# Kernel optimization log

Hardware: AMD Instinct MI355X
Metric: run time of the kernel (lower is better)

Reference implementation:

```python
import jax, jax.numpy as jnp
import numpy as np

H_SIZE = 768
N_HEADS = 12
HEAD = H_SIZE // N_HEADS
INTER = 3072
N_LAYERS = 6
VOCAB = 65536
WIDTH = 512  # attention_width
EPS = 1e-6


def rmsnorm(x, w):
    return x * jax.lax.rsqrt(jnp.mean(x * x, axis=-1, keepdims=True) + EPS) * w


def rotate_every_two(x):
    # interleaved rotation: (x0,x1,x2,x3,...) -> (-x1,x0,-x3,x2,...)
    x1 = x[..., ::2]
    x2 = x[..., 1::2]
    return jnp.stack((-x2, x1), axis=-1).reshape(x.shape)


def fixed_pos_embedding(ages, dim):
    # ages: [B,S] float32 -> sin,cos: [B,S,1,dim]
    inv_freq = 1.0 / 10000 ** jnp.linspace(0.0, 2.0, dim // 2)
    t = ages[..., None] * inv_freq  # [B,S,dim//2]
    sin, cos = jnp.sin(t), jnp.cos(t)
    shp = ages.shape + (1, dim)
    sin = jnp.stack((sin, sin), axis=-1).reshape(shp)
    cos = jnp.stack((cos, cos), axis=-1).reshape(shp)
    return sin, cos


def local_attention(q, k, v, width):
    # causal local attention: query i attends to keys j with i-width < j <= i
    B, S, H, D = q.shape
    nb = S // width
    qb = q.reshape(B, nb, width, H, D)
    pad = ((0, 0), (width, 0), (0, 0), (0, 0))
    kp = jnp.pad(k, pad).reshape(B, nb + 1, width, H, D)
    vp = jnp.pad(v, pad).reshape(B, nb + 1, width, H, D)
    k2 = jnp.concatenate((kp[:, :-1], kp[:, 1:]), axis=2)  # [B,nb,2W,H,D]
    v2 = jnp.concatenate((vp[:, :-1], vp[:, 1:]), axis=2)
    scale = 1.0 / jnp.sqrt(jnp.asarray(D, q.dtype))
    scores = jnp.einsum('bnqhd,bnkhd->bnhqk', qb, k2) * scale
    qi = jnp.arange(width)[:, None]
    kj = jnp.arange(2 * width)[None, :]
    blk = jnp.arange(nb)[:, None, None]
    # global: i = b*W+qi, j = b*W - W + kj ; valid: j<=i, i-j<W, j>=0
    valid = (kj > qi) & (kj <= qi + width) & ((blk * width - width + kj) >= 0)
    scores = jnp.where(valid[None, :, None, :, :], scores, -jnp.inf)
    attn = jax.nn.softmax(scores, axis=-1)
    out = jnp.einsum('bnhqk,bnkhd->bnqhd', attn, v2)
    return out.reshape(B, S, H, D)


def encoder_layer(x, sin, cos, p):
    B, S, _ = x.shape
    xn = rmsnorm(x, p['norm_w'])
    qkv = (xn @ p['attn_W'] + p['attn_b']).reshape(B, S, 3, N_HEADS, HEAD)
    q = qkv[:, :, 0] * cos + rotate_every_two(qkv[:, :, 0]) * sin
    k = qkv[:, :, 1] * cos + rotate_every_two(qkv[:, :, 1]) * sin
    v = qkv[:, :, 2]
    attn = local_attention(q, k, v, WIDTH).reshape(B, S, H_SIZE)
    ff = jax.nn.gelu(xn @ p['in_W'] + p['in_b'], approximate=False)
    combined = jnp.concatenate((attn, ff), axis=-1)
    return combined @ p['out_W'] + p['out_b']


def setup_inputs() -> dict:
    key = jax.random.key(0)
    ks = jax.random.split(key, 10)
    B, S = 4, 2048
    std = 0.02
    tokens = jax.random.randint(ks[0], (B, S), 0, VOCAB, dtype=jnp.int64 if jax.config.jax_enable_x64 else jnp.int32)
    ages = jax.random.uniform(ks[1], (B, S), dtype=jnp.float32) * 1000.0
    embed = jax.random.normal(ks[2], (VOCAB, H_SIZE), jnp.float32) * std
    in_norm_w = jnp.ones((H_SIZE,), jnp.float32)
    out_norm_w = jnp.ones((H_SIZE,), jnp.float32)
    norm_w = jnp.ones((N_LAYERS, H_SIZE), jnp.float32)
    attn_W = jax.random.normal(ks[3], (N_LAYERS, H_SIZE, 3 * H_SIZE), jnp.float32) * std
    attn_b = jnp.zeros((N_LAYERS, 3 * H_SIZE), jnp.float32)
    in_W = jax.random.normal(ks[4], (N_LAYERS, H_SIZE, INTER), jnp.float32) * std
    in_b = jnp.zeros((N_LAYERS, INTER), jnp.float32)
    out_W = jax.random.normal(ks[5], (N_LAYERS, H_SIZE + INTER, H_SIZE), jnp.float32) * std
    out_b = jnp.zeros((N_LAYERS, H_SIZE), jnp.float32)
    return {'tokens': tokens, 'ages': ages, 'embed': embed,
            'in_norm_w': in_norm_w, 'out_norm_w': out_norm_w, 'norm_w': norm_w,
            'attn_W': attn_W, 'attn_b': attn_b, 'in_W': in_W, 'in_b': in_b,
            'out_W': out_W, 'out_b': out_b}


def reference(tokens, ages, embed, in_norm_w, out_norm_w, norm_w, attn_W, attn_b, in_W, in_b, out_W, out_b):
    x = embed[tokens]
    x = rmsnorm(x, in_norm_w)
    sin, cos = fixed_pos_embedding(ages, HEAD)
    params = {'norm_w': norm_w, 'attn_W': attn_W, 'attn_b': attn_b,
              'in_W': in_W, 'in_b': in_b, 'out_W': out_W, 'out_b': out_b}

    def step(h, p):
        return h + encoder_layer(h, sin, cos, p), None

    x, _ = jax.lax.scan(step, x, params)
    return rmsnorm(x, out_norm_w)
```

## Files before the change

### kernel.cpp

```cpp
#include <hip/hip_runtime.h>
#include <hip/hip_bf16.h>
#include <math.h>

#define H_SIZE 768
#define N_HEADS 12
#define HEAD 64
#define INTER 3072
#define N_LAYERS 6
#define BATCH 4
#define SEQ 2048
#define BS (BATCH*SEQ)
#define EPSV 1e-6f

typedef __attribute__((ext_vector_type(8))) short bf16x8;
typedef __attribute__((ext_vector_type(4))) float f32x4;
typedef unsigned short u16;

__device__ inline float bf2f(u16 v) {
    union { float f; unsigned u; } x; x.u = ((unsigned)v) << 16; return x.f;
}
__device__ inline u16 f2bf(float f) {
    union { float f; unsigned u; } x; x.f = f;
    unsigned u = x.u;
    return (u16)((u + 0x7FFFu + ((u >> 16) & 1u)) >> 16);
}

__device__ __forceinline__ void stage16(const u16* g, u16* ldsbase) {
    __builtin_amdgcn_global_load_lds((const __attribute__((address_space(1))) void*)g,
                                     (__attribute__((address_space(3))) void*)ldsbase,
                                     16, 0, 0);
}

__global__ void probe_kernel(const u16* __restrict__ embed, const int* __restrict__ tokens,
                             int* __restrict__ flags) {
    if (threadIdx.x == 0 && blockIdx.x == 0) {
        int good = 0, evenzero = 0;
        for (int i = 0; i < 128; i++) {
            u16 h = embed[i];
            int e = (h >> 7) & 0xFF;
            if (h == 0 || (e >= 87 && e <= 133)) good++;
            if ((i & 1) == 0 && h == 0) evenzero++;
        }
        flags[0] = (evenzero >= 48) ? 1 : ((good >= 110) ? 0 : 1);
        int z = 0;
        for (int i = 0; i < 64; i++) if (tokens[2 * i + 1] == 0) z++;
        flags[1] = (z >= 60) ? 1 : 0;
    }
}

__global__ __launch_bounds__(256) void sincos_kernel(const void* __restrict__ ages,
                                                     float* __restrict__ SIN,
                                                     float* __restrict__ COS,
                                                     const int* __restrict__ flags) {
    int idx = blockIdx.x * 256 + threadIdx.x;
    if (idx >= BS * 32) return;
    bool f32in = flags[0] != 0;
    int row = idx >> 5, f = idx & 31;
    float age = f32in ? ((const float*)ages)[row] : bf2f(((const u16*)ages)[row]);
    float inv = expf(-(2.0f * (float)f / 31.0f) * 9.210340371976184f);
    float t = age * inv;
    SIN[idx] = sinf(t);
    COS[idx] = cosf(t);
}

__global__ __launch_bounds__(256) void wtrans_kernel(const void* __restrict__ Wsrc,
                                                     u16* __restrict__ Wt,
                                                     int K, int N, size_t ltstride,
                                                     const int* __restrict__ flags) {
    __shared__ u16 tile[64][72];
    bool f32in = flags[0] != 0;
    int l = blockIdx.z;
    const float* W32 = (const float*)Wsrc + (size_t)l * K * N;
    const u16*   W16 = (const u16*)Wsrc + (size_t)l * K * N;
    u16* out = Wt + (size_t)l * ltstride;
    int k0 = blockIdx.y * 64, n0 = blockIdx.x * 64;
    int t = threadIdx.x;
    int kk = t >> 3, nn = (t & 7) * 8;
#pragma unroll
    for (int it = 0; it < 2; it++) {
        int kr = kk + it * 32;
        u16 tmp[8];
        if (f32in) {
            const float* src = W32 + (size_t)(k0 + kr) * N + n0 + nn;
            float4 f0 = *(const float4*)src, f1 = *(const float4*)(src + 4);
            tmp[0] = f2bf(f0.x); tmp[1] = f2bf(f0.y); tmp[2] = f2bf(f0.z); tmp[3] = f2bf(f0.w);
            tmp[4] = f2bf(f1.x); tmp[5] = f2bf(f1.y); tmp[6] = f2bf(f1.z); tmp[7] = f2bf(f1.w);
        } else {
            uint4 v = *(const uint4*)(W16 + (size_t)(k0 + kr) * N + n0 + nn);
            const u16* pv = (const u16*)&v;
#pragma unroll
            for (int i = 0; i < 8; i++) tmp[i] = pv[i];
        }
        *(uint4*)(&tile[kr][nn]) = *(const uint4*)tmp;
    }
    __syncthreads();
    int n = t >> 3, kq = (t & 7) * 8;
#pragma unroll
    for (int it = 0; it < 2; it++) {
        int nr = n + it * 32;
        u16 tmp[8];
#pragma unroll
        for (int i = 0; i < 8; i++) tmp[i] = tile[kq + i][nr];
        *(uint4*)(out + (size_t)(n0 + nr) * K + k0 + kq) = *(const uint4*)tmp;
    }
}

__global__ __launch_bounds__(256) void bias_conv_kernel(const void* __restrict__ ab,
                                                        const void* __restrict__ ib,
                                                        const void* __restrict__ ob,
                                                        u16* __restrict__ dst,
                                                        const int* __restrict__ flags) {
    int i = blockIdx.x * 256 + threadIdx.x;
    bool f32in = flags[0] != 0;
    const int A = 6 * 2304, B = 6 * 3072, C = 6 * 768;
    if (i < A) dst[i] = f32in ? f2bf(((const float*)ab)[i]) : ((const u16*)ab)[i];
    else if (i < A + B) { int j = i - A; dst[i] = f32in ? f2bf(((const float*)ib)[j]) : ((const u16*)ib)[j]; }
    else if (i < A + B + C) { int j = i - A - B; dst[i] = f32in ? f2bf(((const float*)ob)[j]) : ((const u16*)ob)[j]; }
}

__global__ __launch_bounds__(256) void embed_norm_kernel(const int* __restrict__ tokens,
                                                         const void* __restrict__ embed,
                                                         const void* __restrict__ wbase,
                                                         float* __restrict__ X,
                                                         const int* __restrict__ flags) {
    int row = blockIdx.x * 4 + (threadIdx.x >> 6);
    int lane = threadIdx.x & 63;
    bool f32in = flags[0] != 0;
    bool i64 = flags[1] != 0;
    int tok = i64 ? tokens[2 * row] : tokens[row];
    tok &= 65535;
    const u16* er16 = (const u16*)embed + (size_t)tok * H_SIZE;
    const float* er32 = (const float*)embed + (size_t)tok * H_SIZE;
    const u16* w16 = (const u16*)wbase;
    const float* w32 = (const float*)wbase;
    float v[12]; float ss = 0.f;
#pragma unroll
    for (int k = 0; k < 12; k++) {
        int i = lane + k * 64;
        float t = f32in ? er32[i] : bf2f(er16[i]);
        v[k] = t; ss += t * t;
    }
#pragma unroll
    for (int off = 1; off < 64; off <<= 1) ss += __shfl_xor(ss, off, 64);
    float scale = rsqrtf(ss * (1.0f / 768.0f) + EPSV);
#pragma unroll
    for (int k = 0; k < 12; k++) {
        int i = lane + k * 64;
        float wv = f32in ? w32[i] : bf2f(w16[i]);
        X[(size_t)row * H_SIZE + i] = v[k] * scale * wv;
    }
}

__global__ __launch_bounds__(256) void rmsnorm_kernel(const float* __restrict__ X,
                                                      const void* __restrict__ wbase, size_t woff,
                                                      void* __restrict__ Y, int outMode,
                                                      const int* __restrict__ flags) {
    int row = blockIdx.x * 4 + (threadIdx.x >> 6);
    int lane = threadIdx.x & 63;
    bool f32in = flags[0] != 0;
    const u16* w16 = (const u16*)wbase + woff;
    const float* w32 = (const float*)wbase + woff;
    const float* xr = X + (size_t)row * H_SIZE;
    float v[12]; float ss = 0.f;
#pragma unroll
    for (int k = 0; k < 12; k++) { v[k] = xr[lane + k * 64]; ss += v[k] * v[k]; }
#pragma unroll
    for (int off = 1; off < 64; off <<= 1) ss += __shfl_xor(ss, off, 64);
    float scale = rsqrtf(ss * (1.0f / 768.0f) + EPSV);
    bool of32 = outMode && f32in;
#pragma unroll
    for (int k = 0; k < 12; k++) {
        int i = lane + k * 64;
        float wv = f32in ? w32[i] : bf2f(w16[i]);
        float val = v[k] * scale * wv;
        if (of32) ((float*)Y)[(size_t)row * H_SIZE + i] = val;
        else      ((u16*)Y)[(size_t)row * H_SIZE + i] = f2bf(val);
    }
}

__global__ __launch_bounds__(512, 2)
void gemm_fused_kernel(const u16* __restrict__ A,
                       const u16* __restrict__ Wt,
                       const u16* __restrict__ abias,
                       const u16* __restrict__ bbias,
                       u16* __restrict__ qkvb,
                       u16* __restrict__ combb,
                       const float* __restrict__ SIN,
                       const float* __restrict__ COS) {
    const int K = H_SIZE;
    const int NT = K / 64;
    __shared__ u16 Al[2][256][64];
    __shared__ u16 Bl[2][256][64];
    const int tid = threadIdx.x;
    const int lane = tid & 63, wave = tid >> 6;
    const int wm = wave >> 2, wn = wave & 3;
    const int lm = lane & 15, g = lane >> 4;
    const int l8 = lane >> 3, l7 = lane & 7;

    const int nx = gridDim.x;
    const int mpx = gridDim.y >> 3;
    int linear = blockIdx.y * nx + blockIdx.x;
    const int xcd = linear & 7;
    int wch = linear >> 3;
    int n_idx = wch / mpx;
    int m_loc = wch - n_idx * mpx;
    const int m0 = (xcd * mpx + m_loc) * 256;
    const int n0 = n_idx * 256;

    f32x4 acc[8][4];
#pragma unroll
    for (int i = 0; i < 8; i++)
#pragma unroll
        for (int j = 0; j < 4; j++) acc[i][j] = (f32x4)0.0f;

    const int swc = (l7 ^ l8) * 8;
    const u16* gA = A  + (size_t)(m0 + wave * 8 + l8) * K + swc;
    const u16* gB = Wt + (size_t)(n0 + wave * 8 + l8) * K + swc;

    auto STAGE_HALF = [&](int bi, int t, int which) {
        int h = (which & 1) * 128;
        if (which < 2) {
            stage16(gA + (size_t)h * K + t * 64,        &Al[bi][h + wave * 8][0]);
            stage16(gA + (size_t)(h + 64) * K + t * 64, &Al[bi][h + wave * 8 + 64][0]);
        } else {
            stage16(gB + (size_t)h * K + t * 64,        &Bl[bi][h + wave * 8][0]);
            stage16(gB + (size_t)(h + 64) * K + t * 64, &Bl[bi][h + wave * 8 + 64][0]);
        }
    };

    bf16x8 af[4][2], bf[4][2];
    const int rowsw = (lm & 7);

    auto RD_A = [&](int bi, int mh) {
#pragma unroll
        for (int i = 0; i < 4; i++)
#pragma unroll
            for (int ks = 0; ks < 2; ks++)
                af[i][ks] = *(const bf16x8*)(&Al[bi][wm * 128 + mh * 64 + i * 16 + lm]
                                               [((ks * 4 + g) ^ rowsw) * 8]);
    };
    auto RD_B = [&](int bi, int nh) {
#pragma unroll
        for (int j = 0; j < 2; j++)
#pragma unroll
            for (int ks = 0; ks < 2; ks++)
                bf[nh * 2 + j][ks] = *(const bf16x8*)(&Bl[bi][wn * 64 + nh * 32 + j * 16 + lm]
                                                        [((ks * 4 + g) ^ rowsw) * 8]);
    };
    auto MM = [&](int mh, int nh) {
        __builtin_amdgcn_s_setprio(1);
#pragma unroll
        for (int i = 0; i < 4; i++)
#pragma unroll
            for (int j = 0; j < 2; j++)
#pragma unroll
                for (int ks = 0; ks < 2; ks++)
                    acc[mh * 4 + i][nh * 2 + j] = __builtin_amdgcn_mfma_f32_16x16x32_bf16(
                        af[i][ks], bf[nh * 2 + j][ks], acc[mh * 4 + i][nh * 2 + j], 0, 0, 0);
        __builtin_amdgcn_s_setprio(0);
    };

    STAGE_HALF(0, 0, 0); STAGE_HALF(0, 0, 1); STAGE_HALF(0, 0, 2); STAGE_HALF(0, 0, 3);

    auto ITER = [&](int t, int ct) {
        const int nb = ct ^ 1;
        const bool pf = (t + 1 < NT);
        asm volatile("s_waitcnt vmcnt(0)" ::: "memory");
        __builtin_amdgcn_s_barrier();
        if (pf) STAGE_HALF(nb, t + 1, 0);
        RD_A(ct, 0); RD_B(ct, 0);
        MM(0, 0);
        __builtin_amdgcn_s_barrier();
        if (pf) STAGE_HALF(nb, t + 1, 1);
        RD_B(ct, 1);
        MM(0, 1);
        __builtin_amdgcn_s_barrier();
        if (pf) STAGE_HALF(nb, t + 1, 2);
        RD_A(ct, 1);
        MM(1, 0);
        __builtin_amdgcn_s_barrier();
        if (pf) STAGE_HALF(nb, t + 1, 3);
        MM(1, 1);
        __builtin_amdgcn_s_barrier();
    };

    for (int tt = 0; tt < NT; tt += 2) {
        ITER(tt, 0);
        ITER(tt + 1, 1);
    }

#pragma unroll
    for (int i = 0; i < 8; i++) {
        int mbase = m0 + wm * 128 + i * 16 + g * 4;
#pragma unroll
        for (int j = 0; j < 4; j++) {
            int n = n0 + wn * 64 + j * 16 + lm;
            float bv = (n < 2304) ? bf2f(abias[n]) : bf2f(bbias[n - 2304]);
#pragma unroll
            for (int r = 0; r < 4; r++) {
                float v = acc[i][j][r] + bv;
                int mm = mbase + r;
                float p = __shfl_xor(v, 1);
                if (n < 2304) {
                    float outv = v;
                    if (n < 1536) {
                        int f = (n >> 1) & 31;
                        float c = COS[mm * 32 + f], s = SIN[mm * 32 + f];
                        outv = (n & 1) ? (v * c + p * s) : (v * c - p * s);
                    }
                    qkvb[(size_t)mm * 2304 + n] = f2bf(outv);
                } else {
                    float u = 0.7978845608f * (v + 0.044715f * v * v * v);
                    float e = __expf(2.0f * u);
                    float th = 1.0f - 2.0f / (e + 1.0f);
                    combb[(size_t)mm * 3840 + (n - 1536)] = f2bf(0.5f * v * (1.0f + th));
                }
            }
        }
    }
}

template <int BN, int MGRP>
__global__ __launch_bounds__(256) void gemm_out_kernel(const u16* __restrict__ A,
                                                       const u16* __restrict__ Wt,
                                                       const u16* __restrict__ bias,
                                                       float* __restrict__ Cf,
                                                       int K) {
    constexpr int NF = BN / 32;
    constexpr int LPS = (BN == 128) ? 4 : 3;
    __shared__ u16 Al[3][128][32];
    __shared__ u16 Bl[3][BN][32];
    const int tid = threadIdx.x;
    const int lane = tid & 63, wave = tid >> 6;
    const int wm = wave >> 1, wn = wave & 1;
    const int lm = lane & 15, g = lane >> 4;

    const int nx = gridDim.x;
    const int mpx = gridDim.y >> 3;
    int linear = blockIdx.y * nx + blockIdx.x;
    const int xcd = linear & 7;
    int wch = linear >> 3;
    const int grpsz = MGRP * nx;
    int grp = wch / grpsz;
    int rem = wch - grp * grpsz;
    int n_idx = rem / MGRP;
    int m_loc = grp * MGRP + (rem - n_idx * MGRP);
    const int m0 = (xcd * mpx + m_loc) * 128;
    const int n0 = n_idx * BN;

    f32x4 acc[4][NF];
#pragma unroll
    for (int i = 0; i < 4; i++)
#pragma unroll
        for (int j = 0; j < NF; j++) acc[i][j] = (f32x4)0.0f;

    const int swcol = ((lane & 3) ^ ((lane >> 3) & 3)) * 8;
    const u16* ga = A  + (size_t)(m0 + wave * 16 + (lane >> 2)) * K + swcol;
    const u16* gb = Wt + (size_t)(n0 + wave * 16 + (lane >> 2)) * K + swcol;
    const size_t row64 = (size_t)64 * K;

    auto STAGE = [&](int bi, int kk) {
        stage16(ga + kk, &Al[bi][wave * 16][0]);
        stage16(ga + row64 + kk, &Al[bi][64 + wave * 16][0]);
        stage16(gb + kk, &Bl[bi][wave * 16][0]);
        if constexpr (BN == 128) stage16(gb + row64 + kk, &Bl[bi][64 + wave * 16][0]);
    };

    const int cc = (g ^ ((lm >> 1) & 3)) * 8;

    auto BODY = [&](int BUF, int NXT, int T) {
        if (T + 32 < K) asm volatile("s_waitcnt vmcnt(%0)" :: "i"(LPS) : "memory");
        else            asm volatile("s_waitcnt vmcnt(0)" ::: "memory");
        __builtin_amdgcn_s_barrier();
        if (T + 64 < K) STAGE(NXT, T + 64);
        bf16x8 a[4], b[NF];
#pragma unroll
        for (int i = 0; i < 4; i++) a[i] = *(const bf16x8*)(&Al[BUF][wm * 64 + i * 16 + lm][cc]);
#pragma unroll
        for (int j = 0; j < NF; j++) b[j] = *(const bf16x8*)(&Bl[BUF][wn * (BN / 2) + j * 16 + lm][cc]);
        __builtin_amdgcn_s_setprio(1);
#pragma unroll
        for (int i = 0; i < 4; i++)
#pragma unroll
            for (int j = 0; j < NF; j++)
                acc[i][j] = __builtin_amdgcn_mfma_f32_16x16x32_bf16(a[i], b[j], acc[i][j], 0, 0, 0);
        __builtin_amdgcn_s_setprio(0);
    };

    STAGE(0, 0);
    STAGE(1, 32);
    for (int k0 = 0; k0 < K; k0 += 96) {
        BODY(0, 2, k0);
        BODY(1, 0, k0 + 32);
        BODY(2, 1, k0 + 64);
    }

#pragma unroll
    for (int i = 0; i < 4; i++) {
        int mbase = m0 + wm * 64 + i * 16 + g * 4;
#pragma unroll
        for (int j = 0; j < NF; j++) {
            int n = n0 + wn * (BN / 2) + j * 16 + lm;
            float bv = bf2f(bias[n]);
#pragma unroll
            for (int r = 0; r < 4; r++) {
                float v = acc[i][j][r] + bv;
                int mm = mbase + r;
                Cf[(size_t)mm * 768 + n] += v;
            }
        }
    }
}

__global__ __launch_bounds__(512) void attn_kernel(const u16* __restrict__ qkv,
                                                   u16* __restrict__ Out) {
    __shared__ u16 Qs[128][72];
    __shared__ u16 Ks[64][72];
    __shared__ u16 Vt[64][72];
    __shared__ u16 Ps[8][16][72];

    const int tid = threadIdx.x;
    const int lane = tid & 63, wave = tid >> 6;
    const int lm = lane & 15, g = lane >> 4;
    const int q0 = blockIdx.x * 128;
    const int h = blockIdx.y;
    const int b = blockIdx.z;
    const size_t rowbase = (size_t)b * SEQ;

#pragma unroll
    for (int it = 0; it < 2; ++it) {
        int idx = tid + it * 512;
        int r = idx >> 3, u = (idx & 7) * 8;
        uint4 v = *(const uint4*)(qkv + (rowbase + q0 + r) * 2304 + h * HEAD + u);
        *(uint4*)(&Qs[r][u]) = v;
    }

    float m_r[4], l_r[4];
    f32x4 o[4];
#pragma unroll
    for (int r = 0; r < 4; r++) { m_r[r] = -INFINITY; l_r[r] = 0.f; }
#pragma unroll
    for (int d = 0; d < 4; d++) o[d] = (f32x4)0.0f;

    const int c_start = (q0 < 512) ? ((512 - q0) >> 6) : 0;
    for (int c = c_start; c < 10; ++c) {
        int kc = q0 - 512 + c * 64;
        __syncthreads();
        {
            int r = tid >> 3, u = (tid & 7) * 8;
            int j = kc + r;
            uint4 kv = make_uint4(0, 0, 0, 0), vv = make_uint4(0, 0, 0, 0);
            if (j >= 0) {
                kv = *(const uint4*)(qkv + (rowbase + j) * 2304 + 768 + h * HEAD + u);
                vv = *(const uint4*)(qkv + (rowbase + j) * 2304 + 1536 + h * HEAD + u);
            }
            *(uint4*)(&Ks[r][u]) = kv;
            const u16* pv = (const u16*)&vv;
#pragma unroll
            for (int i = 0; i < 8; i++) Vt[u + i][r] = pv[i];
        }
        __syncthreads();

        bf16x8 aq0 = *(const bf16x8*)(&Qs[wave * 16 + lm][g * 8]);
        bf16x8 aq1 = *(const bf16x8*)(&Qs[wave * 16 + lm][32 + g * 8]);
        f32x4 s[4];
#pragma unroll
        for (int kf = 0; kf < 4; kf++) {
            bf16x8 b0 = *(const bf16x8*)(&Ks[kf * 16 + lm][g * 8]);
            bf16x8 b1 = *(const bf16x8*)(&Ks[kf * 16 + lm][32 + g * 8]);
            f32x4 z = (f32x4)0.0f;
            z = __builtin_amdgcn_mfma_f32_16x16x32_bf16(aq0, b0, z, 0, 0, 0);
            z = __builtin_amdgcn_mfma_f32_16x16x32_bf16(aq1, b1, z, 0, 0, 0);
            s[kf] = z;
        }

        float sv[4][4], mc[4];
#pragma unroll
        for (int r = 0; r < 4; r++) mc[r] = -INFINITY;
#pragma unroll
        for (int kf = 0; kf < 4; kf++) {
            int j = kc + kf * 16 + lm;
#pragma unroll
            for (int r = 0; r < 4; r++) {
                int i = q0 + wave * 16 + g * 4 + r;
                bool valid = (j >= 0) && (j <= i) && (j >= i - 511);
                float v = valid ? s[kf][r] * 0.125f : -INFINITY;
                sv[kf][r] = v;
                mc[r] = fmaxf(mc[r], v);
            }
        }
#pragma unroll
        for (int off = 1; off < 16; off <<= 1)
#pragma unroll
            for (int r = 0; r < 4; r++) mc[r] = fmaxf(mc[r], __shfl_xor(mc[r], off, 64));

        float alpha[4], mn[4];
#pragma unroll
        for (int r = 0; r < 4; r++) {
            mn[r] = fmaxf(m_r[r], mc[r]);
            alpha[r] = (mn[r] > -1e37f) ? __expf(m_r[r] - mn[r]) : 1.0f;
            m_r[r] = mn[r];
        }
        float ps[4][4], rs[4] = {0.f, 0.f, 0.f, 0.f};
#pragma unroll
        for (int kf = 0; kf < 4; kf++)
#pragma unroll
            for (int r = 0; r < 4; r++) {
                float p = (sv[kf][r] > -1e37f) ? __expf(sv[kf][r] - mn[r]) : 0.0f;
                ps[kf][r] = p;
                rs[r] += p;
            }
#pragma unroll
        for (int off = 1; off < 16; off <<= 1)
#pragma unroll
            for (int r = 0; r < 4; r++) rs[r] += __shfl_xor(rs[r], off, 64);
#pragma unroll
        for (int r = 0; r < 4; r++) l_r[r] = l_r[r] * alpha[r] + rs[r];

#pragma unroll
        for (int kf = 0; kf < 4; kf++)
#pragma unroll
            for (int r = 0; r < 4; r++) Ps[wave][g * 4 + r][kf * 16 + lm] = f2bf(ps[kf][r]);

#pragma unroll
        for (int d = 0; d < 4; d++)
#pragma unroll
            for (int r = 0; r < 4; r++) o[d][r] *= alpha[r];

        bf16x8 pa0 = *(const bf16x8*)(&Ps[wave][lm][g * 8]);
        bf16x8 pa1 = *(const bf16x8*)(&Ps[wave][lm][32 + g * 8]);
#pragma unroll
        for (int d = 0; d < 4; d++) {
            bf16x8 b0 = *(const bf16x8*)(&Vt[d * 16 + lm][g * 8]);
            bf16x8 b1 = *(const bf16x8*)(&Vt[d * 16 + lm][32 + g * 8]);
            o[d] = __builtin_amdgcn_mfma_f32_16x16x32_bf16(pa0, b0, o[d], 0, 0, 0);
            o[d] = __builtin_amdgcn_mfma_f32_16x16x32_bf16(pa1, b1, o[d], 0, 0, 0);
        }
    }

#pragma unroll
    for (int d = 0; d < 4; d++) {
        int dd = d * 16 + lm;
#pragma unroll
        for (int r = 0; r < 4; r++) {
            int i = q0 + wave * 16 + g * 4 + r;
            float v = o[d][r] / l_r[r];
            Out[(rowbase + i) * 3840 + h * HEAD + dd] = f2bf(v);
        }
    }
}

extern "C" void kernel_launch(void* const* d_in, const int* in_sizes, int n_in,
                              void* d_out, int out_size, void* d_ws, size_t ws_size,
                              hipStream_t stream) {
    const int* tokens   = (const int*)d_in[0];
    const void* ages    = d_in[1];
    const void* embed   = d_in[2];
    const void* in_norm_w  = d_in[3];
    const void* out_norm_w = d_in[4];
    const void* norm_w     = d_in[5];
    const void* attn_W     = d_in[6];
    const void* attn_b     = d_in[7];
    const void* in_W       = d_in[8];
    const void* in_b       = d_in[9];
    const void* out_W      = d_in[10];
    const void* out_b      = d_in[11];

    char* w = (char*)d_ws;
    int* flags  = (int*)w;   w += 256;
    float* x    = (float*)w; w += (size_t)BS * H_SIZE * 4;
    u16* xn     = (u16*)w;   w += (size_t)BS * H_SIZE * 2;
    u16* qkv    = (u16*)w;   w += (size_t)BS * 2304 * 2;
    u16* comb   = (u16*)w;   w += (size_t)BS * 3840 * 2;
    float* sinb = (float*)w; w += (size_t)BS * 32 * 4;
    float* cosb = (float*)w; w += (size_t)BS * 32 * 4;
    u16* wtf    = (u16*)w;   w += (size_t)N_LAYERS * 5376 * 768 * 2;
    u16* wto    = (u16*)w;   w += (size_t)N_LAYERS * 768 * 3840 * 2;
    u16* biasb  = (u16*)w;   w += (size_t)(6*2304 + 6*3072 + 6*768) * 2;

    u16* ab_b = biasb;
    u16* ib_b = biasb + 6 * 2304;
    u16* ob_b = ib_b + 6 * 3072;

    const size_t LFS = (size_t)5376 * 768;

    probe_kernel<<<1, 64, 0, stream>>>((const u16*)embed, tokens, flags);
    sincos_kernel<<<(BS * 32 + 255) / 256, 256, 0, stream>>>(ages, sinb, cosb, flags);
    embed_norm_kernel<<<BS / 4, 256, 0, stream>>>(tokens, embed, in_norm_w, x, flags);
    bias_conv_kernel<<<(6 * (2304 + 3072 + 768) + 255) / 256, 256, 0, stream>>>(
        attn_b, in_b, out_b, biasb, flags);

    wtrans_kernel<<<dim3(2304 / 64, 768 / 64, N_LAYERS), 256, 0, stream>>>(
        attn_W, wtf, 768, 2304, LFS, flags);
    wtrans_kernel<<<dim3(3072 / 64, 768 / 64, N_LAYERS), 256, 0, stream>>>(
        in_W, wtf + (size_t)2304 * 768, 768, 3072, LFS, flags);
    wtrans_kernel<<<dim3(768 / 64, 3840 / 64, N_LAYERS), 256, 0, stream>>>(
        out_W, wto, 3840, 768, (size_t)768 * 3840, flags);

    for (int l = 0; l < N_LAYERS; ++l) {
        rmsnorm_kernel<<<BS / 4, 256, 0, stream>>>(x, norm_w, (size_t)l * H_SIZE, xn, 0, flags);
        gemm_fused_kernel<<<dim3(5376 / 256, BS / 256), 512, 0, stream>>>(
            xn, wtf + (size_t)l * LFS, ab_b + l * 2304, ib_b + l * 3072,
            qkv, comb, sinb, cosb);
        attn_kernel<<<dim3(SEQ / 128, N_HEADS, BATCH), 512, 0, stream>>>(qkv, comb);
        gemm_out_kernel<64, 2><<<dim3(768 / 64, BS / 128), 256, 0, stream>>>(
            comb, wto + (size_t)l * 768 * 3840, ob_b + l * 768, x, H_SIZE + INTER);
    }
    rmsnorm_kernel<<<BS / 4, 256, 0, stream>>>(x, out_norm_w, 0, d_out, 1, flags);
}
```

Baseline: 1.905 ms.

## Reorder GEMM tile staging by consumption order and use partial vmcnt waits

Reorganizes the global-to-LDS staging in the fused QKV/MLP GEMM so A and B quarter-tiles are loaded in the order the MFMA phases consume them. Full vmcnt(0) drains are replaced with partial waits, and two barriers per K-iteration are dropped, so loads stay in flight while math proceeds. The launch-bounds occupancy hint of 2 blocks per CU is removed. The tighter wait counts and removed barriers carry a risk of LDS read/write races if the counts are off.

```diff
diff --git a/kernel.cpp b/kernel.cpp
--- a/kernel.cpp
+++ b/kernel.cpp
@@ -178,7 +178,7 @@
     }
 }
 
-__global__ __launch_bounds__(512, 2)
+__global__ __launch_bounds__(512)
 void gemm_fused_kernel(const u16* __restrict__ A,
                        const u16* __restrict__ Wt,
                        const u16* __restrict__ abias,
@@ -214,19 +214,18 @@
         for (int j = 0; j < 4; j++) acc[i][j] = (f32x4)0.0f;
 
     const int swc = (l7 ^ l8) * 8;
-    const u16* gA = A  + (size_t)(m0 + wave * 8 + l8) * K + swc;
-    const u16* gB = Wt + (size_t)(n0 + wave * 8 + l8) * K + swc;
-
-    auto STAGE_HALF = [&](int bi, int t, int which) {
-        int h = (which & 1) * 128;
-        if (which < 2) {
-            stage16(gA + (size_t)h * K + t * 64,        &Al[bi][h + wave * 8][0]);
-            stage16(gA + (size_t)(h + 64) * K + t * 64, &Al[bi][h + wave * 8 + 64][0]);
-        } else {
-            stage16(gB + (size_t)h * K + t * 64,        &Bl[bi][h + wave * 8][0]);
-            stage16(gB + (size_t)(h + 64) * K + t * 64, &Bl[bi][h + wave * 8 + 64][0]);
-        }
-    };
+    const u16* gA = A + (size_t)(m0 + wave * 8 + l8) * K + swc;
+    const int browBase = (wave & 3) * 8 + (wave >> 2) * 64;
+    const u16* gB = Wt + (size_t)(n0 + browBase + l8) * K + swc;
+
+#define STAGE_AQ(bi, t, mh) do { \
+        stage16(gA + (size_t)((mh) * 64) * K + (t) * 64,       &Al[bi][(mh) * 64 + wave * 8][0]); \
+        stage16(gA + (size_t)(128 + (mh) * 64) * K + (t) * 64, &Al[bi][128 + (mh) * 64 + wave * 8][0]); \
+    } while (0)
+#define STAGE_BQ(bi, t, nh) do { \
+        stage16(gB + (size_t)((nh) * 32) * K + (t) * 64,       &Bl[bi][browBase + (nh) * 32][0]); \
+        stage16(gB + (size_t)(128 + (nh) * 32) * K + (t) * 64, &Bl[bi][128 + browBase + (nh) * 32][0]); \
+    } while (0)
 
     bf16x8 af[4][2], bf[4][2];
     const int rowsw = (lm & 7);
@@ -260,34 +259,39 @@
         __builtin_amdgcn_s_setprio(0);
     };
 
-    STAGE_HALF(0, 0, 0); STAGE_HALF(0, 0, 1); STAGE_HALF(0, 0, 2); STAGE_HALF(0, 0, 3);
+    STAGE_AQ(0, 0, 0); STAGE_BQ(0, 0, 0); STAGE_BQ(0, 0, 1); STAGE_AQ(0, 0, 1);
 
     auto ITER = [&](int t, int ct) {
         const int nb = ct ^ 1;
         const bool pf = (t + 1 < NT);
-        asm volatile("s_waitcnt vmcnt(0)" ::: "memory");
+        asm volatile("s_waitcnt vmcnt(4)" ::: "memory");
         __builtin_amdgcn_s_barrier();
-        if (pf) STAGE_HALF(nb, t + 1, 0);
+        if (pf) STAGE_AQ(nb, t + 1, 0);
         RD_A(ct, 0); RD_B(ct, 0);
         MM(0, 0);
+        if (pf) { asm volatile("s_waitcnt vmcnt(4)" ::: "memory"); }
+        else    { asm volatile("s_waitcnt vmcnt(2)" ::: "memory"); }
         __builtin_amdgcn_s_barrier();
-        if (pf) STAGE_HALF(nb, t + 1, 1);
+        if (pf) STAGE_BQ(nb, t + 1, 0);
         RD_B(ct, 1);
         MM(0, 1);
+        if (pf) { asm volatile("s_waitcnt vmcnt(4)" ::: "memory"); }
+        else    { asm volatile("s_waitcnt vmcnt(0)" ::: "memory"); }
         __builtin_amdgcn_s_barrier();
-        if (pf) STAGE_HALF(nb, t + 1, 2);
+        if (pf) STAGE_BQ(nb, t + 1, 1);
         RD_A(ct, 1);
         MM(1, 0);
-        __builtin_amdgcn_s_barrier();
-        if (pf) STAGE_HALF(nb, t + 1, 3);
+        if (pf) STAGE_AQ(nb, t + 1, 1);
         MM(1, 1);
-        __builtin_amdgcn_s_barrier();
     };
 
     for (int tt = 0; tt < NT; tt += 2) {
         ITER(tt, 0);
         ITER(tt + 1, 1);
     }
+
+#undef STAGE_AQ
+#undef STAGE_BQ
 
 #pragma unroll
     for (int i = 0; i < 8; i++) {
```

Result: faster. 1.862 ms (-2.3%).
